# Performance work log

Measured on AMD Instinct MI355X. Metric: run time of the kernel, lower is better.

## Reference

```python
import jax, jax.numpy as jnp
import numpy as np

S0, P0 = 4096, 64      # level0 segments, points per level0 segment
S1, P1 = 1024, 256     # level1 superpoints, points per level1 segment
C = 128                # feature dim
KNN = 3                # K (neighbor_range=1 -> 3 candidates)
N = S0 * P0


def setup_inputs() -> dict:
    key = jax.random.key(0)
    ks = jax.random.split(key, 8)
    return {
        "sp_center_feat": jax.random.normal(ks[0], (S1, C), jnp.float32),
        "sp_center_coord": jax.random.normal(ks[1], (S1, 3), jnp.float32),
        "rawPoint_feat": jax.random.normal(ks[2], (N, C), jnp.float32),
        "hilbert_feat_coord": jax.random.normal(ks[3], (N, 3), jnp.float32),
        "points_feat": jax.random.normal(ks[4], (S0, P0, C), jnp.float32),
        "points_coord": jax.random.normal(ks[5], (S0, P0, 3), jnp.float32),
        "level0_to_level1_indices": jnp.sort(jax.random.randint(ks[6], (S0,), 0, S1)).astype(jnp.int64),
        "num_segments0": S0,
        "points_per_segment0": P0,
        "num_segments1": S1,
        "points_per_segment1": P1,
        "K": KNN,
    }


def reference(sp_center_feat, sp_center_coord, rawPoint_feat, hilbert_feat_coord,
              points_feat, points_coord, level0_to_level1_indices,
              num_segments0, points_per_segment0, num_segments1, points_per_segment1, K):
    # --- neighbor superpoint candidates (neighbor_range = 1) ---
    offsets = jnp.arange(-1, 2)                                        # [3]
    nb = jnp.clip(jnp.arange(num_segments0)[:, None] + offsets[None, :], 0, num_segments0 - 1)  # [S0,3]
    sp_idx = level0_to_level1_indices[nb]                              # [S0,3]
    nb_feat = sp_center_feat[sp_idx]                                   # [S0,3,C]
    nb_coord = sp_center_coord[sp_idx]                                 # [S0,3,3]

    # --- cdist + topk (smallest K) ---
    diff = points_coord[:, :, None, :] - nb_coord[:, None, :, :]       # [S0,P0,3,3]
    dist = jnp.sqrt(jnp.maximum(jnp.sum(diff * diff, axis=-1), 0.0))   # [S0,P0,3]
    _, knn_idx = jax.lax.top_k(-dist, K)                               # [S0,P0,K], ascending distance

    # --- gather neighbor feats, dot-product similarity, softmax, argmax ---
    b = jnp.arange(num_segments0)[:, None, None]
    knn_sp_feats = nb_feat[b, knn_idx]                                 # [S0,P0,K,C]
    sim = jnp.einsum('spc,spkc->spk', points_feat, knn_sp_feats)       # [S0,P0,K]
    sim = jax.nn.softmax(sim, axis=-1)
    max_idx = jnp.argmax(sim, axis=-1)                                 # [S0,P0]

    # --- map winning neighbor slot -> superpoint id ---
    sp_knn = sp_idx[b, knn_idx]                                        # [S0,P0,K]
    assigned = jnp.take_along_axis(sp_knn, max_idx[..., None], axis=2)[..., 0]  # [S0,P0]
    point_assignments = assigned.reshape(-1)                           # [N]

    # cross_attention_update_sp is empty -> sp_center_feat passes through unchanged

    # --- scatter-mean: new superpoint centers ---
    seg_sum = jax.ops.segment_sum(hilbert_feat_coord, point_assignments, num_segments=num_segments1)
    counts = jax.ops.segment_sum(jnp.ones((point_assignments.shape[0],), hilbert_feat_coord.dtype),
                                 point_assignments, num_segments=num_segments1)
    new_sp_center_coord = seg_sum / jnp.maximum(counts, 1.0)[:, None]  # [S1,3]

    feat_dim = rawPoint_feat.shape[-1]
    hilbert_feat_level1 = rawPoint_feat.reshape(num_segments1, points_per_segment1, feat_dim)
    points_feat_out = rawPoint_feat.reshape(num_segments0, points_per_segment0, feat_dim)

    return (point_assignments, sp_center_feat, new_sp_center_coord, points_feat_out, hilbert_feat_level1)
```

## Files before the change

kernel.cpp:

```cpp
#include <hip/hip_runtime.h>

#define S0 4096
#define P0 64
#define S1 1024
#define P1 256
#define C  128
#define N_PTS (S0 * P0)

#define SEG_PER_BLK   4
#define ASSIGN_BLOCKS (S0 / SEG_PER_BLK)
#define TOTAL_BLOCKS  2048

__global__ __launch_bounds__(256) void fused_kernel(
    const float* __restrict__ sp_feat,
    const float* __restrict__ pts_feat,
    const float* __restrict__ hilb,
    const int*   __restrict__ l01,
    const float4* __restrict__ raw,
    float*  __restrict__ out_assign,
    float4* __restrict__ o_pf,
    float4* __restrict__ o_h1,
    float4* __restrict__ o_spf,
    float*  __restrict__ ws_sum,
    float*  __restrict__ ws_cnt)
{
    __shared__ float lsum[4][3][3];
    __shared__ float lcnt[4][3];

    const int tid  = threadIdx.x;
    const int blk  = blockIdx.x;
    const int w    = tid >> 6;
    const int lane = tid & 63;

    if (blk < ASSIGN_BLOCKS) {
        if (tid < 36) ((float*)lsum)[tid] = 0.0f;
        if (tid < 12) ((float*)lcnt)[tid] = 0.0f;
        __syncthreads();

        const int s  = blk * SEG_PER_BLK + w;
        const int sm = (s - 1 < 0) ? 0 : s - 1;
        const int sp = (s + 1 >= S0) ? S0 - 1 : s + 1;
        const int id0 = l01[sm], id1 = l01[s], id2 = l01[sp];

        const int h = lane >> 5;
        const int q = (lane & 31) * 4;

        const float4 c0 = *reinterpret_cast<const float4*>(sp_feat + (size_t)id0 * C + q);
        const float4 c1 = *reinterpret_cast<const float4*>(sp_feat + (size_t)id1 * C + q);
        const float4 c2 = *reinterpret_cast<const float4*>(sp_feat + (size_t)id2 * C + q);

        const float* segb = pts_feat + (size_t)s * P0 * C;

        #pragma unroll 4
        for (int k = 0; k < 32; ++k) {
            const int row = 2 * k + h;
            float4 v = *reinterpret_cast<const float4*>(segb + (size_t)row * C + q);
            float p0 = v.x * c0.x + v.y * c0.y + v.z * c0.z + v.w * c0.w;
            float p1 = v.x * c1.x + v.y * c1.y + v.z * c1.z + v.w * c1.w;
            float p2 = v.x * c2.x + v.y * c2.y + v.z * c2.z + v.w * c2.w;
            #pragma unroll
            for (int off = 1; off < 32; off <<= 1) {
                p0 += __shfl_xor(p0, off);
                p1 += __shfl_xor(p1, off);
                p2 += __shfl_xor(p2, off);
            }
            if ((lane & 31) == 0) {
                int kb = 0; float best = p0;
                if (p1 > best) { best = p1; kb = 1; }
                if (p2 > best) { best = p2; kb = 2; }
                const int gpt = s * P0 + row;
                out_assign[gpt] = (float)(kb == 0 ? id0 : (kb == 1 ? id1 : id2));
                const float* hp = hilb + (size_t)gpt * 3;
                atomicAdd(&lsum[w][kb][0], hp[0]);
                atomicAdd(&lsum[w][kb][1], hp[1]);
                atomicAdd(&lsum[w][kb][2], hp[2]);
                atomicAdd(&lcnt[w][kb], 1.0f);
            }
        }
        __syncthreads();

        if (tid < 12) {
            const int ww = tid >> 2;
        }
        if (tid < 12) {
            const int ww = tid / 3, kb = tid % 3;
            if (lcnt[ww][kb] > 0.0f) {
                const int s2 = blk * SEG_PER_BLK + ww;
                int nb = s2 - 1 + kb;
                nb = nb < 0 ? 0 : (nb >= S0 ? S0 - 1 : nb);
                const int id = l01[nb];
                atomicAdd(&ws_cnt[id], lcnt[ww][kb]);
                atomicAdd(&ws_sum[(size_t)id * 3 + 0], lsum[ww][kb][0]);
                atomicAdd(&ws_sum[(size_t)id * 3 + 1], lsum[ww][kb][1]);
                atomicAdd(&ws_sum[(size_t)id * 3 + 2], lsum[ww][kb][2]);
            }
        }
    }

    const long NR = (long)N_PTS * C / 4;
    const long NS = (long)S1 * C / 4;
    const long gid    = (long)blk * 256 + tid;
    const long stride = (long)TOTAL_BLOCKS * 256;
    const float4* spf4 = (const float4*)sp_feat;
    for (long i = gid; i < NR; i += stride) {
        float4 v = raw[i];
        o_pf[i] = v;
        o_h1[i] = v;
        if (i < NS) o_spf[i] = spf4[i];
    }
}

__global__ void finalize_kernel(const float* __restrict__ ws_sum,
                                const float* __restrict__ ws_cnt,
                                float* __restrict__ out_coord)
{
    int i = blockIdx.x * blockDim.x + threadIdx.x;
    if (i >= S1 * 3) return;
    out_coord[i] = ws_sum[i] / fmaxf(ws_cnt[i / 3], 1.0f);
}

extern "C" void kernel_launch(void* const* d_in, const int* in_sizes, int n_in,
                              void* d_out, int out_size, void* d_ws, size_t ws_size,
                              hipStream_t stream) {
    const float* sp_feat  = (const float*)d_in[0];
    const float* raw      = (const float*)d_in[2];
    const float* hilb     = (const float*)d_in[3];
    const float* pts_feat = (const float*)d_in[4];
    const int*   l01      = (const int*)d_in[6];

    float* out        = (float*)d_out;
    float* out_assign = out;
    float* out_spfeat = out_assign + N_PTS;
    float* out_coord  = out_spfeat + (size_t)S1 * C;
    float* out_pf     = out_coord + (size_t)S1 * 3;
    float* out_h1     = out_pf + (size_t)S0 * P0 * C;

    float* ws_sum = (float*)d_ws;
    float* ws_cnt = ws_sum + (size_t)S1 * 3;

    hipMemsetAsync(d_ws, 0, (size_t)(S1 * 3 + S1) * sizeof(float), stream);

    fused_kernel<<<TOTAL_BLOCKS, 256, 0, stream>>>(
        sp_feat, pts_feat, hilb, l01, (const float4*)raw,
        out_assign, (float4*)out_pf, (float4*)out_h1, (float4*)out_spfeat,
        ws_sum, ws_cnt);

    finalize_kernel<<<(S1 * 3 + 255) / 256, 256, 0, stream>>>(ws_sum, ws_cnt, out_coord);
}
```

Before: 127.2 us.

## Fuse finalize into main kernel via last-block counter, nontemporal unrolled copy

```diff
diff --git a/kernel.cpp b/kernel.cpp
--- a/kernel.cpp
+++ b/kernel.cpp
@@ -1,4 +1,6 @@
 #include <hip/hip_runtime.h>
+
+typedef float f32x4 __attribute__((ext_vector_type(4)));
 
 #define S0 4096
 #define P0 64
@@ -10,22 +12,29 @@
 #define SEG_PER_BLK   4
 #define ASSIGN_BLOCKS (S0 / SEG_PER_BLK)
 #define TOTAL_BLOCKS  2048
+#define NR            ((long)N_PTS * C / 4)
+#define NS            ((long)S1 * C / 4)
+#define CPY_STRIDE    ((long)TOTAL_BLOCKS * 256)
+#define UNROLL        8
 
 __global__ __launch_bounds__(256) void fused_kernel(
     const float* __restrict__ sp_feat,
     const float* __restrict__ pts_feat,
     const float* __restrict__ hilb,
     const int*   __restrict__ l01,
-    const float4* __restrict__ raw,
+    const f32x4* __restrict__ raw,
     float*  __restrict__ out_assign,
-    float4* __restrict__ o_pf,
-    float4* __restrict__ o_h1,
-    float4* __restrict__ o_spf,
+    f32x4*  __restrict__ o_pf,
+    f32x4*  __restrict__ o_h1,
+    f32x4*  __restrict__ o_spf,
+    float*  __restrict__ out_coord,
     float*  __restrict__ ws_sum,
-    float*  __restrict__ ws_cnt)
+    float*  __restrict__ ws_cnt,
+    unsigned* __restrict__ ws_done)
 {
     __shared__ float lsum[4][3][3];
     __shared__ float lcnt[4][3];
+    __shared__ int   last_flag;
 
     const int tid  = threadIdx.x;
     const int blk  = blockIdx.x;
@@ -45,16 +54,17 @@
         const int h = lane >> 5;
         const int q = (lane & 31) * 4;
 
-        const float4 c0 = *reinterpret_cast<const float4*>(sp_feat + (size_t)id0 * C + q);
-        const float4 c1 = *reinterpret_cast<const float4*>(sp_feat + (size_t)id1 * C + q);
-        const float4 c2 = *reinterpret_cast<const float4*>(sp_feat + (size_t)id2 * C + q);
+        const f32x4 c0 = *reinterpret_cast<const f32x4*>(sp_feat + (size_t)id0 * C + q);
+        const f32x4 c1 = *reinterpret_cast<const f32x4*>(sp_feat + (size_t)id1 * C + q);
+        const f32x4 c2 = *reinterpret_cast<const f32x4*>(sp_feat + (size_t)id2 * C + q);
 
         const float* segb = pts_feat + (size_t)s * P0 * C;
 
         #pragma unroll 4
         for (int k = 0; k < 32; ++k) {
             const int row = 2 * k + h;
-            float4 v = *reinterpret_cast<const float4*>(segb + (size_t)row * C + q);
+            f32x4 v = __builtin_nontemporal_load(
+                reinterpret_cast<const f32x4*>(segb + (size_t)row * C + q));
             float p0 = v.x * c0.x + v.y * c0.y + v.z * c0.z + v.w * c0.w;
             float p1 = v.x * c1.x + v.y * c1.y + v.z * c1.z + v.w * c1.w;
             float p2 = v.x * c2.x + v.y * c2.y + v.z * c2.z + v.w * c2.w;
@@ -80,9 +90,6 @@
         __syncthreads();
 
         if (tid < 12) {
-            const int ww = tid >> 2;
-        }
-        if (tid < 12) {
             const int ww = tid / 3, kb = tid % 3;
             if (lcnt[ww][kb] > 0.0f) {
                 const int s2 = blk * SEG_PER_BLK + ww;
@@ -95,28 +102,42 @@
                 atomicAdd(&ws_sum[(size_t)id * 3 + 2], lsum[ww][kb][2]);
             }
         }
+        __syncthreads();
+
+        if (tid == 0) {
+            __threadfence();
+            last_flag = (atomicAdd(ws_done, 1u) == ASSIGN_BLOCKS - 1) ? 1 : 0;
+        }
+        __syncthreads();
+        if (last_flag) {
+            for (int i = tid; i < S1 * 3; i += 256) {
+                float sv = atomicAdd(&ws_sum[i], 0.0f);
+                float cv = atomicAdd(&ws_cnt[i / 3], 0.0f);
+                out_coord[i] = sv / fmaxf(cv, 1.0f);
+            }
+        }
     }
 
-    const long NR = (long)N_PTS * C / 4;
-    const long NS = (long)S1 * C / 4;
-    const long gid    = (long)blk * 256 + tid;
-    const long stride = (long)TOTAL_BLOCKS * 256;
-    const float4* spf4 = (const float4*)sp_feat;
-    for (long i = gid; i < NR; i += stride) {
-        float4 v = raw[i];
-        o_pf[i] = v;
-        o_h1[i] = v;
-        if (i < NS) o_spf[i] = spf4[i];
+    const long gid = (long)blk * 256 + tid;
+    if (gid < NS) o_spf[gid] = ((const f32x4*)sp_feat)[gid];
+
+    f32x4* __restrict__ A = (blk & 1) ? o_h1 : o_pf;
+    f32x4* __restrict__ B = (blk & 1) ? o_pf : o_h1;
+
+    #pragma unroll
+    for (int batch = 0; batch < 2; ++batch) {
+        f32x4 v[UNROLL];
+        #pragma unroll
+        for (int t = 0; t < UNROLL; ++t)
+            v[t] = __builtin_nontemporal_load(
+                &raw[gid + (long)(batch * UNROLL + t) * CPY_STRIDE]);
+        #pragma unroll
+        for (int t = 0; t < UNROLL; ++t) {
+            const long i = gid + (long)(batch * UNROLL + t) * CPY_STRIDE;
+            __builtin_nontemporal_store(v[t], &A[i]);
+            __builtin_nontemporal_store(v[t], &B[i]);
+        }
     }
-}
-
-__global__ void finalize_kernel(const float* __restrict__ ws_sum,
-                                const float* __restrict__ ws_cnt,
-                                float* __restrict__ out_coord)
-{
-    int i = blockIdx.x * blockDim.x + threadIdx.x;
-    if (i >= S1 * 3) return;
-    out_coord[i] = ws_sum[i] / fmaxf(ws_cnt[i / 3], 1.0f);
 }
 
 extern "C" void kernel_launch(void* const* d_in, const int* in_sizes, int n_in,
@@ -135,15 +156,14 @@
     float* out_pf     = out_coord + (size_t)S1 * 3;
     float* out_h1     = out_pf + (size_t)S0 * P0 * C;
 
-    float* ws_sum = (float*)d_ws;
-    float* ws_cnt = ws_sum + (size_t)S1 * 3;
+    float*    ws_sum  = (float*)d_ws;
+    float*    ws_cnt  = ws_sum + (size_t)S1 * 3;
+    unsigned* ws_done = (unsigned*)(ws_cnt + S1);
 
-    hipMemsetAsync(d_ws, 0, (size_t)(S1 * 3 + S1) * sizeof(float), stream);
+    (void)hipMemsetAsync(d_ws, 0, (size_t)(S1 * 3 + S1 + 1) * sizeof(float), stream);
 
     fused_kernel<<<TOTAL_BLOCKS, 256, 0, stream>>>(
-        sp_feat, pts_feat, hilb, l01, (const float4*)raw,
-        out_assign, (float4*)out_pf, (float4*)out_h1, (float4*)out_spfeat,
-        ws_sum, ws_cnt);
-
-    finalize_kernel<<<(S1 * 3 + 255) / 256, 256, 0, stream>>>(ws_sum, ws_cnt, out_coord);
+        sp_feat, pts_feat, hilb, l01, (const f32x4*)raw,
+        out_assign, (f32x4*)out_pf, (f32x4*)out_h1, (f32x4*)out_spfeat,
+        out_coord, ws_sum, ws_cnt, ws_done);
 }
```

Measured after the change: 190.2 us. 1.5x slower.
